# Kernel tuning notes

Measured on AMD Instinct MI355X. Metric: run time of the kernel, lower is better.

## Reference

```python
import jax, jax.numpy as jnp
import numpy as np
from jax import lax

SR = 4      # sr_ratio
HEADS = 8   # num_heads


def _upsample_bilinear_ac(x, out_h, out_w):
    # torch nn.Upsample(scale_factor=SR, mode='bilinear', align_corners=True)
    B, C, h, w = x.shape
    ys = jnp.linspace(0.0, h - 1.0, out_h)
    xs = jnp.linspace(0.0, w - 1.0, out_w)
    y0 = jnp.floor(ys).astype(jnp.int32)
    y1 = jnp.minimum(y0 + 1, h - 1)
    wy = (ys - y0).astype(x.dtype)
    x0 = jnp.floor(xs).astype(jnp.int32)
    x1 = jnp.minimum(x0 + 1, w - 1)
    wx = (xs - x0).astype(x.dtype)
    r = x[:, :, y0, :] * (1.0 - wy)[None, None, :, None] + x[:, :, y1, :] * wy[None, None, :, None]
    return r[:, :, :, x0] * (1.0 - wx) + r[:, :, :, x1] * wx


def _forward(x, sr_w, sr_b, ln_g, ln_b, q_w, k1_w, v1_w, k2_w, v2_w, proj_w, proj_b):
    B, C, H, W = x.shape
    ID = C // 4                      # internal_dim
    hd = ID // HEADS                 # head_dim
    scale = float(hd) ** -0.5
    # spatial-reduction conv for Q path: [B, ID, H/4, W/4]
    qf = lax.conv_general_dilated(x, sr_w, (SR, SR), 'VALID',
                                  dimension_numbers=('NCHW', 'OIHW', 'NCHW'))
    qf = qf + sr_b[None, :, None, None]
    Hs, Ws = qf.shape[2], qf.shape[3]
    N = Hs * Ws
    qf = qf.reshape(B, ID, N).transpose(0, 2, 1)          # [B, N, ID]
    # LayerNorm
    mu = qf.mean(-1, keepdims=True)
    var = qf.var(-1, keepdims=True)
    qn = (qf - mu) / jnp.sqrt(var + 1e-5) * ln_g + ln_b
    q = qn @ q_w                                          # [B, N, ID]
    # max / avg pooled K,V inputs: [B, N, C]
    xm = lax.reduce_window(x, -jnp.inf, lax.max, (1, 1, SR, SR), (1, 1, SR, SR), 'VALID')
    xm = xm.reshape(B, C, N).transpose(0, 2, 1)
    xa = lax.reduce_window(x, 0.0, lax.add, (1, 1, SR, SR), (1, 1, SR, SR), 'VALID') / float(SR * SR)
    xa = xa.reshape(B, C, N).transpose(0, 2, 1)

    def heads(t):
        return t.reshape(B, N, HEADS, hd).transpose(0, 2, 1, 3)  # [B, H, N, hd]

    qh = heads(q)
    k1, v1 = heads(xm @ k1_w), heads(xm @ v1_w)
    k2, v2 = heads(xa @ k2_w), heads(xa @ v2_w)

    def attend(k, v):
        a = jax.nn.softmax(jnp.einsum('bhnd,bhmd->bhnm', qh, k) * scale, axis=-1)
        return jnp.einsum('bhnm,bhmd->bhnd', a, v)

    z = attend(k1, v1) + attend(k2, v2)                   # [B, H, N, hd]
    z = z.transpose(0, 2, 1, 3).reshape(B, N, ID)
    z = z @ proj_w + proj_b                               # [B, N, C]
    z = z.transpose(0, 2, 1).reshape(B, C, Hs, Ws)
    return _upsample_bilinear_ac(z, H, W)


def setup_inputs() -> dict:
    key = jax.random.key(0)
    ks = jax.random.split(key, 9)
    B, C, H, W = 16, 256, 112, 112
    ID = C // 4

    def n(k, shape, s=0.02):
        return jax.random.normal(k, shape, jnp.float32) * s

    return {
        'x': jax.random.normal(ks[0], (B, C, H, W), jnp.float32),
        'sr_w': n(ks[1], (ID, C, SR, SR)),
        'sr_b': jnp.zeros((ID,), jnp.float32),
        'ln_g': jnp.ones((ID,), jnp.float32),
        'ln_b': jnp.zeros((ID,), jnp.float32),
        'q_w': n(ks[2], (ID, ID)),
        'k1_w': n(ks[3], (C, ID)),
        'v1_w': n(ks[4], (C, ID)),
        'k2_w': n(ks[5], (C, ID)),
        'v2_w': n(ks[6], (C, ID)),
        'proj_w': n(ks[7], (ID, C)),
        'proj_b': jnp.zeros((C,), jnp.float32),
    }


def reference(x, sr_w, sr_b, ln_g, ln_b, q_w, k1_w, v1_w, k2_w, v2_w, proj_w, proj_b):
    return _forward(x, sr_w, sr_b, ln_g, ln_b, q_w, k1_w, v1_w, k2_w, v2_w, proj_w, proj_b)
```

## Files before the change

kernel.cpp:

```cpp
#include <hip/hip_runtime.h>
#include <math.h>

typedef __attribute__((ext_vector_type(8))) short short8;
typedef __attribute__((ext_vector_type(4))) short bh4;
typedef __attribute__((ext_vector_type(4))) float f32x4;
typedef __attribute__((ext_vector_type(2))) unsigned uint2v;
typedef __attribute__((ext_vector_type(4))) unsigned uint4v;

#define MFMA16(A,B,C) __builtin_amdgcn_mfma_f32_16x16x32_bf16(A,B,C,0,0,0)

#if __has_builtin(__builtin_amdgcn_mfma_f32_16x16x16bf16_1k)
#define MFMA16x16(A,B,C) __builtin_amdgcn_mfma_f32_16x16x16bf16_1k(A,B,C,0,0,0)
#else
__device__ __forceinline__ f32x4 mfma16x16_asm(bh4 a, bh4 b, f32x4 c){
    asm volatile("v_mfma_f32_16x16x16_bf16 %0, %1, %2, %0" : "+v"(c) : "v"(a), "v"(b));
    return c;
}
#define MFMA16x16(A,B,C) mfma16x16_asm(A,B,C)
#endif

__device__ __forceinline__ unsigned short f2b(float f){
    unsigned u = __builtin_bit_cast(unsigned, f);
    return (unsigned short)((u + 0x7fffu + ((u>>16)&1u)) >> 16);
}
__device__ __forceinline__ unsigned pk2(float a, float b){
    return (unsigned)f2b(a) | ((unsigned)f2b(b) << 16);
}
__device__ __forceinline__ unsigned pk2rn(float a, float b){
    unsigned ua = __builtin_bit_cast(unsigned, a) + 0x8000u;
    unsigned ub = __builtin_bit_cast(unsigned, b) + 0x8000u;
    return (ua >> 16) | (ub & 0xffff0000u);
}
__device__ __forceinline__ void gl_lds16(const void* g, void* l){
    __builtin_amdgcn_global_load_lds(
        (const __attribute__((address_space(1))) void*)g,
        (__attribute__((address_space(3))) void*)l, 16, 0, 0);
}


__global__ __launch_bounds__(256) void ktw(const float* __restrict__ srw,
    const float* __restrict__ qw, const float* __restrict__ k1w,
    const float* __restrict__ v1w, const float* __restrict__ k2w,
    const float* __restrict__ v2w, char* __restrict__ srwb,
    char* __restrict__ Wtm, char* __restrict__ Wta, char* __restrict__ QWt)
{
    int blk = blockIdx.x, t = threadIdx.x;
    if (blk < 128){
        int base = blk*2048 + t*8;
        float4 a = *(const float4*)(srw + base);
        float4 b = *(const float4*)(srw + base + 4);
        uint4 u = { pk2(a.x,a.y), pk2(a.z,a.w), pk2(b.x,b.y), pk2(b.z,b.w) };
        *(uint4*)(srwb + (size_t)base*2) = u;
    } else if (blk < 136){
        __shared__ float T[256*33];
        int idx = blk - 128, fi = idx >> 1, half = idx & 1;
        const float* src = (fi==0) ? k1w : (fi==1) ? v1w : (fi==2) ? k2w : v2w;
        char* dst = ((fi < 2) ? Wtm : Wta) + (size_t)((fi & 1)*64 + half*32) * 512;
        for (int li = t; li < 8192; li += 256){
            int c = li >> 5, o = li & 31;
            T[c*33 + o] = src[c*64 + half*32 + o];
        }
        __syncthreads();
        for (int lo = t; lo < 1024; lo += 256){
            int o = lo >> 5, c8 = lo & 31;
            float v[8];
            #pragma unroll
            for (int k = 0; k < 8; ++k) v[k] = T[(c8*8 + k)*33 + o];
            uint4 u = { pk2(v[0],v[1]), pk2(v[2],v[3]), pk2(v[4],v[5]), pk2(v[6],v[7]) };
            *(uint4*)(dst + o*512 + c8*16) = u;
        }
    } else {
        __shared__ float T[64*65];
        for (int li = t; li < 4096; li += 256)
            T[(li >> 6)*65 + (li & 63)] = qw[li];
        __syncthreads();
        for (int lo = t; lo < 512; lo += 256){
            int o = lo >> 3, i8 = lo & 7;
            float v[8];
            #pragma unroll
            for (int k = 0; k < 8; ++k) v[k] = T[(i8*8 + k)*65 + o];
            uint4 u = { pk2(v[0],v[1]), pk2(v[2],v[3]), pk2(v[4],v[5]), pk2(v[6],v[7]) };
            *(uint4*)(QWt + o*128 + i8*16) = u;
        }
    }
}

__global__ __launch_bounds__(256) void k1(const float* __restrict__ x,
    const char* __restrict__ srwb, char* __restrict__ R, float* __restrict__ pws)
{
    __shared__ __align__(16) char Xb0[14336];
    __shared__ __align__(16) char Xb1[14336];
    __shared__ __align__(16) char Xb2[14336];
    __shared__ unsigned pmpa[28*66];
    int blk = blockIdx.x;
    int b = blk / 112, r5 = blk % 112, hs = r5 >> 2, cg4 = r5 & 3;
    int t = threadIdx.x;
    int w = t >> 6, l = t & 63, lr = l & 15, lg = l >> 4;
    int p0 = lr, p1m = min(16 + lr, 27);
    int nIss = (w < 3) ? 4 : 2;
    int jbase = (w < 3) ? w*4 : 12;

    size_t gchunk[4]; int ldso[4];
    #pragma unroll
    for (int q = 0; q < 4; ++q){
        int byte_in = (jbase + q)*1024 + l*16;
        int c = byte_in / 1792, rem = byte_in - c*1792;
        gchunk[q] = (size_t)c*50176 + rem;
        ldso[q] = (jbase + q)*1024;
    }
    const char* xstage = (const char*)x
        + ((size_t)(b*256 + cg4*64)*12544 + (size_t)hs*448)*4;
    const char* bRow = srwb + (size_t)(w*16 + lr)*8192 + cg4*2048 + lg*16;
    int pl_p = t >> 3, pl_c = t & 7;

    f32x4 acc0 = {0.f,0.f,0.f,0.f}, acc1 = {0.f,0.f,0.f,0.f};
    short8 Q00,Q01,Q02,Q03, Q10,Q11,Q12,Q13, Q20,Q21,Q22,Q23;

#define BPRE(B0,B1,B2,B3,S) do{ \
    B0 = *(const short8*)(bRow + (S)*256);      \
    B1 = *(const short8*)(bRow + (S)*256 + 64); \
    B2 = *(const short8*)(bRow + (S)*256 + 128);\
    B3 = *(const short8*)(bRow + (S)*256 + 192); }while(0)

#define STAGE(XB,S) do{ \
    const char* _gb = xstage + (size_t)(S)*401408; \
    _Pragma("unroll") for (int q = 0; q < 4; ++q){ \
        if (q < nIss) gl_lds16(_gb + gchunk[q], XB + ldso[q]); } }while(0)

#define WAIT16 do{ if (w < 3) asm volatile("s_waitcnt vmcnt(16)" ::: "memory"); \
                   else       asm volatile("s_waitcnt vmcnt(12)" ::: "memory"); \
                   __builtin_amdgcn_sched_barrier(0); }while(0)
#define WAIT8  do{ if (w < 3) asm volatile("s_waitcnt vmcnt(8)" ::: "memory"); \
                   else       asm volatile("s_waitcnt vmcnt(6)" ::: "memory"); \
                   __builtin_amdgcn_sched_barrier(0); }while(0)
#define WAIT0  do{ asm volatile("s_waitcnt vmcnt(0)" ::: "memory"); \
                   __builtin_amdgcn_sched_barrier(0); }while(0)
#define BAR    do{ __builtin_amdgcn_s_barrier(); __builtin_amdgcn_sched_barrier(0); }while(0)

#define COMP(XB,B0,B1,B2,B3,S) do{ \
    if (t < 224){ \
        const char* cb = XB + pl_c*1792 + pl_p*16; \
        f32x4 r0 = *(const f32x4*)(cb);        f32x4 r1 = *(const f32x4*)(cb + 448); \
        f32x4 r2 = *(const f32x4*)(cb + 896);  f32x4 r3 = *(const f32x4*)(cb + 1344); \
        float mx = fmaxf(fmaxf(fmaxf(r0[0],r0[1]),fmaxf(r0[2],r0[3])), \
                         fmaxf(fmaxf(r1[0],r1[1]),fmaxf(r1[2],r1[3]))); \
        mx = fmaxf(mx, fmaxf(fmaxf(fmaxf(r2[0],r2[1]),fmaxf(r2[2],r2[3])), \
                             fmaxf(fmaxf(r3[0],r3[1]),fmaxf(r3[2],r3[3])))); \
        float sm = ((r0[0]+r0[1])+(r0[2]+r0[3])) + ((r1[0]+r1[1])+(r1[2]+r1[3])) \
                 + ((r2[0]+r2[1])+(r2[2]+r2[3])) + ((r3[0]+r3[1])+(r3[2]+r3[3])); \
        pmpa[pl_p*66 + (S)*8 + pl_c] = pk2(mx, sm * (1.f/16.f)); \
    } \
    _Pragma("unroll") for (int ks = 0; ks < 4; ++ks){ \
        const char* abase = XB + (ks*2 + (lg>>1))*1792 + (lg&1)*896; \
        f32x4 lo0 = *(const f32x4*)(abase + p0*16); \
        f32x4 hi0 = *(const f32x4*)(abase + 448 + p0*16); \
        f32x4 lo1 = *(const f32x4*)(abase + p1m*16); \
        f32x4 hi1 = *(const f32x4*)(abase + 448 + p1m*16); \
        short8 af0 = __builtin_bit_cast(short8, \
            (uint4v){ pk2(lo0[0],lo0[1]), pk2(lo0[2],lo0[3]), pk2(hi0[0],hi0[1]), pk2(hi0[2],hi0[3]) }); \
        short8 af1 = __builtin_bit_cast(short8, \
            (uint4v){ pk2(lo1[0],lo1[1]), pk2(lo1[2],lo1[3]), pk2(hi1[0],hi1[1]), pk2(hi1[2],hi1[3]) }); \
        short8 bq = (ks==0)?B0:(ks==1)?B1:(ks==2)?B2:B3; \
        acc0 = MFMA16(af0, bq, acc0); \
        acc1 = MFMA16(af1, bq, acc1); } }while(0)

    BPRE(Q00,Q01,Q02,Q03, 0); STAGE(Xb0, 0);
    BPRE(Q10,Q11,Q12,Q13, 1); STAGE(Xb1, 1);
    BPRE(Q20,Q21,Q22,Q23, 2); STAGE(Xb2, 2);

    WAIT16; BAR; COMP(Xb0, Q00,Q01,Q02,Q03, 0); BAR;
    BPRE(Q00,Q01,Q02,Q03, 3); STAGE(Xb0, 3);
    WAIT16; BAR; COMP(Xb1, Q10,Q11,Q12,Q13, 1); BAR;
    BPRE(Q10,Q11,Q12,Q13, 4); STAGE(Xb1, 4);
    WAIT16; BAR; COMP(Xb2, Q20,Q21,Q22,Q23, 2); BAR;
    BPRE(Q20,Q21,Q22,Q23, 5); STAGE(Xb2, 5);
    WAIT16; BAR; COMP(Xb0, Q00,Q01,Q02,Q03, 3); BAR;
    BPRE(Q00,Q01,Q02,Q03, 6); STAGE(Xb0, 6);
    WAIT16; BAR; COMP(Xb1, Q10,Q11,Q12,Q13, 4); BAR;
    BPRE(Q10,Q11,Q12,Q13, 7); STAGE(Xb1, 7);
    WAIT16; BAR; COMP(Xb2, Q20,Q21,Q22,Q23, 5); BAR;
    WAIT8;  BAR; COMP(Xb0, Q00,Q01,Q02,Q03, 6); BAR;
    WAIT0;  BAR; COMP(Xb1, Q10,Q11,Q12,Q13, 7);

#undef BPRE
#undef STAGE
#undef WAIT16
#undef WAIT8
#undef WAIT0
#undef BAR
#undef COMP

    size_t rowB = (size_t)b*784 + hs*28;
    float* pp = pws + (size_t)((b*28 + hs)*4 + cg4)*1792;
    #pragma unroll
    for (int rg = 0; rg < 4; ++rg){
        int m0 = lg*4 + rg, m1 = 16 + lg*4 + rg;
        pp[m0*64 + w*16 + lr] = acc0[rg];
        if (m1 < 28) pp[m1*64 + w*16 + lr] = acc1[rg];
    }
    __syncthreads();
    if (t < 224){
        int m = t >> 3, sub = t & 7;
        unsigned u[8];
        #pragma unroll
        for (int k = 0; k < 8; ++k) u[k] = pmpa[m*66 + sub*8 + k];
        uint4 um = { (u[0]&0xffffu)|(u[1]<<16), (u[2]&0xffffu)|(u[3]<<16),
                     (u[4]&0xffffu)|(u[5]<<16), (u[6]&0xffffu)|(u[7]<<16) };
        uint4 ua = { (u[0]>>16)|(u[1]&0xffff0000u), (u[2]>>16)|(u[3]&0xffff0000u),
                     (u[4]>>16)|(u[5]&0xffff0000u), (u[6]>>16)|(u[7]&0xffff0000u) };
        *(uint4*)(R + (rowB + m)*1024 + cg4*128 + sub*16)       = um;
        *(uint4*)(R + (rowB + m)*1024 + 512 + cg4*128 + sub*16) = ua;
    }
}

__global__ __launch_bounds__(512) void k2(const float* __restrict__ pws_,
    const float* __restrict__ srb, const float* __restrict__ lng,
    const float* __restrict__ lnb, const char* __restrict__ Wtm,
    const char* __restrict__ Wta, const char* __restrict__ QWt,
    char* __restrict__ R)
{
    __shared__ __align__(16) char PM[16384];
    __shared__ __align__(16) char PA[16384];
    __shared__ float Db[32*64];
    __shared__ __align__(16) char QN[4096];
    int blk = blockIdx.x, b = blk/28, hs = blk%28;
    int t = threadIdx.x, w = t>>6, l = t&63, lr = l&15, lg = l>>4;
    size_t rowB = (size_t)b*784 + hs*28;
    const char* Rb = R + rowB*1024;
    for (int li = t; li < 896; li += 512){
        int m = li >> 5, c16 = li & 31;
        uint4 vm = *(const uint4*)(Rb + (size_t)m*1024 + c16*16);
        uint4 va = *(const uint4*)(Rb + (size_t)m*1024 + 512 + c16*16);
        int dst = m*512 + ((c16*16) ^ ((m&7)<<4));
        *(uint4*)(PM + dst) = vm;
        *(uint4*)(PA + dst) = va;
    }
    const float* p0 = pws_ + (size_t)(b*28 + hs)*4*1792;
    for (int e = t; e < 1792; e += 512)
        Db[e] = ((p0[e] + p0[1792+e]) + (p0[3584+e] + p0[5376+e])) + srb[e & 63];
    __syncthreads();
    float g = lng[l], be = lnb[l];
    #pragma unroll
    for (int i = 0; i < 4; ++i){
        int m = w + i*8;
        float v = Db[m*64 + l];
        float s = v, ss = v*v;
        #pragma unroll
        for (int off = 1; off < 64; off <<= 1){
            s  += __shfl_xor(s,  off, 64);
            ss += __shfl_xor(ss, off, 64);
        }
        float mu = s * (1.f/64.f);
        float var = ss * (1.f/64.f) - mu*mu;
        float qn = (v - mu) * rsqrtf(var + 1e-5f) * g + be;
        *(unsigned short*)(QN + m*128 + ((l*2) ^ ((m&7)<<4))) = f2b(qn);
    }
    __syncthreads();
    int fam = w >> 2, ofp = w & 3;
    const char* PMA = fam ? PA : PM;
    const char* Wt  = fam ? Wta : Wtm;
    f32x4 a00={0.f,0.f,0.f,0.f}, a01=a00, a10=a00, a11=a00;
    int swzr = (lr & 7) << 4;
    #pragma unroll
    for (int ks = 0; ks < 8; ++ks){
        int kb = ks*64 + lg*16;
        short8 x0 = *(const short8*)(PMA + lr*512 + (kb ^ swzr));
        short8 x1 = *(const short8*)(PMA + (16+lr)*512 + (kb ^ swzr));
        short8 b0 = *(const short8*)(Wt + (size_t)(ofp*32 + lr)*512 + kb);
        short8 b1 = *(const short8*)(Wt + (size_t)(ofp*32 + 16 + lr)*512 + kb);
        a00 = MFMA16(x0, b0, a00); a01 = MFMA16(x0, b1, a01);
        a10 = MFMA16(x1, b0, a10); a11 = MFMA16(x1, b1, a11);
    }
    f32x4 q0={0.f,0.f,0.f,0.f}, q1=q0;
    if (w < 4){
        #pragma unroll
        for (int ks = 0; ks < 2; ++ks){
            int kb = ks*64 + lg*16;
            short8 xa_ = *(const short8*)(QN + lr*128 + (kb ^ swzr));
            short8 xb_ = *(const short8*)(QN + (16+lr)*128 + (kb ^ swzr));
            short8 bq  = *(const short8*)(QWt + (size_t)(w*16 + lr)*128 + kb);
            q0 = MFMA16(xa_, bq, q0);
            q1 = MFMA16(xb_, bq, q1);
        }
    }
    #pragma unroll
    for (int j = 0; j < 2; ++j){
        int o128 = ofp*32 + j*16 + lr;
        int o = o128 & 63, hh = o >> 3, dd = o & 7, mat = fam*2 + (o128 >> 6);
        int byteoff = 128 + hh*64 + mat*16 + dd*2;
        f32x4 am  = j ? a01 : a00;
        f32x4 am1 = j ? a11 : a10;
        #pragma unroll
        for (int rg = 0; rg < 4; ++rg){
            int m0 = lg*4 + rg, m1 = 16 + lg*4 + rg;
            *(unsigned short*)(R + (rowB + m0)*1024 + byteoff) = f2b(am[rg]);
            if (m1 < 28)
                *(unsigned short*)(R + (rowB + m1)*1024 + byteoff) = f2b(am1[rg]);
        }
    }
    if (w < 4){
        int o = w*16 + lr;
        #pragma unroll
        for (int rg = 0; rg < 4; ++rg){
            int m0 = lg*4 + rg, m1 = 16 + lg*4 + rg;
            *(unsigned short*)(R + (rowB + m0)*1024 + o*2) = f2b(q0[rg]);
            if (m1 < 28)
                *(unsigned short*)(R + (rowB + m1)*1024 + o*2) = f2b(q1[rg]);
        }
    }
}

__global__ __launch_bounds__(256) void kattn(const char* __restrict__ R, float* __restrict__ z)
{
    __shared__ __align__(16) char QT [6144];
    __shared__ __align__(16) char K1b[5376];
    __shared__ __align__(16) char K2b[5376];
    __shared__ __align__(16) char VT1[3840];
    __shared__ __align__(16) char VT2[3840];
    int blk = blockIdx.x;
    int bh = blk / 7, nseg = blk % 7;
    int b = bh >> 3, h = bh & 7;
    int t = threadIdx.x, w = t >> 6, l = t & 63;
    int col = l & 15, g = l >> 4;

    for (int i = t; i < 384; i += 256) ((uint4*)QT)[i] = uint4{0,0,0,0};
    for (int i = t; i < 112; i += 256){
        *(uint4*)(K1b + i*48 + 16) = uint4{0,0,0,0};
        *(uint4*)(K2b + i*48 + 16) = uint4{0,0,0,0};
    }
    for (int i = t; i < 120; i += 256){
        *(uint4*)(VT1 + 1920 + i*16) = uint4{0,0,0,0};
        *(uint4*)(VT2 + 1920 + i*16) = uint4{0,0,0,0};
    }
    __syncthreads();
    if (t < 112){
        uint4 qv = *(const uint4*)(R + ((size_t)b*784 + nseg*112 + t)*1024 + h*16);
        *(uint2*)(QT + t*48)     = uint2{qv.x, qv.y};
        *(uint2*)(QT + t*48 + 8) = uint2{qv.z, qv.w};
    }
    __syncthreads();

    bh4 qf[2];
    #pragma unroll
    for (int nf = 0; nf < 2; ++nf)
        qf[nf] = *(const bh4*)(QT + (w*28 + nf*16 + col)*48 + g*8);

    f32x4 o1[2] = {{0,0,0,0},{0,0,0,0}}, o2[2] = {{0,0,0,0},{0,0,0,0}};
    float d1[2] = {0.f,0.f}, d2[2] = {0.f,0.f};
    const float C2 = 0.51004244f;

    for (int mt = 0; mt < 7; ++mt){
        __syncthreads();
        for (int li = t; li < 448; li += 256){
            int m = li >> 2, part = li & 3;
            uint4 v = *(const uint4*)(R + ((size_t)b*784 + mt*112 + m)*1024 + 128 + h*64 + part*16);
            if ((part & 1) == 0){
                char* Kb = (part == 0) ? K1b : K2b;
                *(uint2*)(Kb + m*48)     = uint2{v.x, v.y};
                *(uint2*)(Kb + m*48 + 8) = uint2{v.z, v.w};
            } else {
                char* Vb = (part == 1) ? VT1 : VT2;
                unsigned arr[4] = {v.x, v.y, v.z, v.w};
                #pragma unroll
                for (int d = 0; d < 4; ++d){
                    *(unsigned short*)(Vb + (d*2)*240   + m*2) = (unsigned short)(arr[d] & 0xffffu);
                    *(unsigned short*)(Vb + (d*2+1)*240 + m*2) = (unsigned short)(arr[d] >> 16);
                }
            }
        }
        __syncthreads();
        #pragma unroll
        for (int mc = 0; mc < 7; ++mc){
            bh4 ka = *(const bh4*)(K1b + (mc*16 + col)*48 + g*8);
            bh4 kb = *(const bh4*)(K2b + (mc*16 + col)*48 + g*8);
            bh4 va = *(const bh4*)(VT1 + col*240 + mc*32 + g*8);
            bh4 vb = *(const bh4*)(VT2 + col*240 + mc*32 + g*8);
            #pragma unroll
            for (int nf = 0; nf < 2; ++nf){
                f32x4 zr = {0.f,0.f,0.f,0.f};
                f32x4 s1 = MFMA16x16(ka, qf[nf], zr);
                float p0 = exp2f(s1[0]*C2), p1 = exp2f(s1[1]*C2);
                float p2 = exp2f(s1[2]*C2), p3 = exp2f(s1[3]*C2);
                d1[nf] += (p0+p1)+(p2+p3);
                bh4 pf1 = __builtin_bit_cast(bh4, (uint2v){pk2rn(p0,p1), pk2rn(p2,p3)});
                o1[nf] = MFMA16x16(va, pf1, o1[nf]);
                f32x4 s2 = MFMA16x16(kb, qf[nf], zr);
                float r0 = exp2f(s2[0]*C2), r1 = exp2f(s2[1]*C2);
                float r2 = exp2f(s2[2]*C2), r3 = exp2f(s2[3]*C2);
                d2[nf] += (r0+r1)+(r2+r3);
                bh4 pf2 = __builtin_bit_cast(bh4, (uint2v){pk2rn(r0,r1), pk2rn(r2,r3)});
                o2[nf] = MFMA16x16(vb, pf2, o2[nf]);
            }
        }
    }
    #pragma unroll
    for (int nf = 0; nf < 2; ++nf){
        d1[nf] += __shfl_xor(d1[nf], 16, 64); d1[nf] += __shfl_xor(d1[nf], 32, 64);
        d2[nf] += __shfl_xor(d2[nf], 16, 64); d2[nf] += __shfl_xor(d2[nf], 32, 64);
    }
    if (g < 2){
        #pragma unroll
        for (int nf = 0; nf < 2; ++nf){
            if (nf == 1 && col >= 12) continue;
            int n = nseg*112 + w*28 + nf*16 + col;
            float ra = 1.f / d1[nf], rb = 1.f / d2[nf];
            float4 ov;
            ov.x = o1[nf][0]*ra + o2[nf][0]*rb;
            ov.y = o1[nf][1]*ra + o2[nf][1]*rb;
            ov.z = o1[nf][2]*ra + o2[nf][2]*rb;
            ov.w = o1[nf][3]*ra + o2[nf][3]*rb;
            *(float4*)(z + ((size_t)b*784 + n)*64 + h*8 + g*4) = ov;
        }
    }
}

__global__ __launch_bounds__(256) void kpu(const float* __restrict__ z,
    const float* __restrict__ pw, const float* __restrict__ pb,
    float* __restrict__ out)
{
    __shared__ float plane[8*784];
    __shared__ float wsl[64*8];
    __shared__ int   ti0[112];
    __shared__ float twv[112];
    int blk = blockIdx.x;
    int b = blk >> 5, cg = blk & 31;
    int t = threadIdx.x;
    if (t < 128){
        #pragma unroll
        for (int q = 0; q < 4; ++q){
            int idx = t*4 + q; int o = idx >> 3, j = idx & 7;
            wsl[o*8 + j] = pw[o*256 + cg*8 + j];
        }
    }
    if (t < 112){
        float s = (float)t * (27.f/111.f);
        int i0 = (int)s; if (i0 > 27) i0 = 27;
        ti0[t] = i0; twv[t] = s - (float)i0;
    }
    __syncthreads();
    {
        int nh = t >> 1, jh = (t & 1) * 4;
        float bias0 = pb[cg*8 + jh], bias1 = pb[cg*8 + jh + 1];
        float bias2 = pb[cg*8 + jh + 2], bias3 = pb[cg*8 + jh + 3];
        for (int n = nh; n < 784; n += 128){
            const float* zr = z + ((size_t)b*784 + n)*64;
            float a0 = bias0, a1 = bias1, a2 = bias2, a3 = bias3;
            #pragma unroll
            for (int o4 = 0; o4 < 16; ++o4){
                float4 zv = *(const float4*)(zr + o4*4);
                const float* wr = wsl + (o4*4)*8 + jh;
                a0 = fmaf(zv.x, wr[0],  a0); a1 = fmaf(zv.x, wr[1],  a1);
                a2 = fmaf(zv.x, wr[2],  a2); a3 = fmaf(zv.x, wr[3],  a3);
                a0 = fmaf(zv.y, wr[8],  a0); a1 = fmaf(zv.y, wr[9],  a1);
                a2 = fmaf(zv.y, wr[10], a2); a3 = fmaf(zv.y, wr[11], a3);
                a0 = fmaf(zv.z, wr[16], a0); a1 = fmaf(zv.z, wr[17], a1);
                a2 = fmaf(zv.z, wr[18], a2); a3 = fmaf(zv.z, wr[19], a3);
                a0 = fmaf(zv.w, wr[24], a0); a1 = fmaf(zv.w, wr[25], a1);
                a2 = fmaf(zv.w, wr[26], a2); a3 = fmaf(zv.w, wr[27], a3);
            }
            plane[(jh+0)*784 + n] = a0;
            plane[(jh+1)*784 + n] = a1;
            plane[(jh+2)*784 + n] = a2;
            plane[(jh+3)*784 + n] = a3;
        }
    }
    __syncthreads();
    float* ob = out + ((size_t)b*256 + cg*8)*12544;
    for (int i = t; i < 12544; i += 256){
        int y = i/112, xx = i%112;
        int y0 = ti0[y], x0 = ti0[xx];
        float wy = twv[y], wx = twv[xx];
        int y1 = min(y0+1, 27), x1 = min(x0+1, 27);
        int i00 = y0*28 + x0, i01 = y0*28 + x1, i10 = y1*28 + x0, i11 = y1*28 + x1;
        #pragma unroll
        for (int j = 0; j < 8; ++j){
            const float* pl = plane + j*784;
            float a  = pl[i00] + (pl[i10]-pl[i00])*wy;
            float bb = pl[i01] + (pl[i11]-pl[i01])*wy;
            ob[(size_t)j*12544 + i] = a + (bb-a)*wx;
        }
    }
}

extern "C" void kernel_launch(void* const* d_in, const int* in_sizes, int n_in,
                              void* d_out, int out_size, void* d_ws, size_t ws_size,
                              hipStream_t stream) {
    const float* x   = (const float*)d_in[0];
    const float* srw = (const float*)d_in[1];
    const float* srb = (const float*)d_in[2];
    const float* lng = (const float*)d_in[3];
    const float* lnb = (const float*)d_in[4];
    const float* qw  = (const float*)d_in[5];
    const float* k1w = (const float*)d_in[6];
    const float* v1w = (const float*)d_in[7];
    const float* k2w = (const float*)d_in[8];
    const float* v2w = (const float*)d_in[9];
    const float* pw  = (const float*)d_in[10];
    const float* pb  = (const float*)d_in[11];

    char*  Rws  = (char*)d_ws;
    float* pws  = (float*)(Rws + 12845056);
    char*  srwb = Rws + 25690112;
    char*  Wtm  = Rws + 26214400;
    char*  Wta  = Rws + 26279936;
    char*  QWt  = Rws + 26345472;
    float* z    = (float*)(Rws + 12845056);
    float* out  = (float*)d_out;

    ktw  <<<137,  256, 0, stream>>>(srw, qw, k1w, v1w, k2w, v2w, srwb, Wtm, Wta, QWt);
    k1   <<<1792, 256, 0, stream>>>(x, srwb, Rws, pws);
    k2   <<<448,  512, 0, stream>>>(pws, srb, lng, lnb, Wtm, Wta, QWt, Rws);
    kattn<<<896,  256, 0, stream>>>(Rws, z);
    kpu  <<<512,  256, 0, stream>>>(z, pw, pb, out);
}
```

Before: 233.6 us.

## Split k1 conv reduction across waves and XOR-swizzle LDS staging

Each wave in k1 now handles one K-slice (two channels) for all 64 output channels, instead of all K-slices for 16 output channels. Each wave does 8 MFMAs per stage from one A-fragment load, which cuts redundant LDS A reads and bf16 conversions. The global-to-LDS layout gets an XOR swizzle on the 16-byte column to reduce LDS bank conflicts. The cost is four times as many accumulator registers, and the per-wave partial sums must be reduced through LDS with extra barriers before the store.

```diff
diff --git a/kernel.cpp b/kernel.cpp
--- a/kernel.cpp
+++ b/kernel.cpp
@@ -88,9 +88,7 @@
 __global__ __launch_bounds__(256) void k1(const float* __restrict__ x,
     const char* __restrict__ srwb, char* __restrict__ R, float* __restrict__ pws)
 {
-    __shared__ __align__(16) char Xb0[14336];
-    __shared__ __align__(16) char Xb1[14336];
-    __shared__ __align__(16) char Xb2[14336];
+    __shared__ __align__(16) char Xb[3][14336];
     __shared__ unsigned pmpa[28*66];
     int blk = blockIdx.x;
     int b = blk / 112, r5 = blk % 112, hs = r5 >> 2, cg4 = r5 & 3;
@@ -105,27 +103,34 @@
     for (int q = 0; q < 4; ++q){
         int byte_in = (jbase + q)*1024 + l*16;
         int c = byte_in / 1792, rem = byte_in - c*1792;
-        gchunk[q] = (size_t)c*50176 + rem;
+        gchunk[q] = (size_t)c*50176 + (size_t)(rem ^ ((c & 7) << 4));
         ldso[q] = (jbase + q)*1024;
     }
     const char* xstage = (const char*)x
         + ((size_t)(b*256 + cg4*64)*12544 + (size_t)hs*448)*4;
-    const char* bRow = srwb + (size_t)(w*16 + lr)*8192 + cg4*2048 + lg*16;
+    const char* bBase = srwb + (size_t)lr*8192 + cg4*2048 + w*64 + lg*16;
     int pl_p = t >> 3, pl_c = t & 7;
-
-    f32x4 acc0 = {0.f,0.f,0.f,0.f}, acc1 = {0.f,0.f,0.f,0.f};
-    short8 Q00,Q01,Q02,Q03, Q10,Q11,Q12,Q13, Q20,Q21,Q22,Q23;
+    int kxp = pl_c << 4;
+    int chA = 2*w + (lg >> 1);
+    int kxA = chA << 4;
+    int remA0 = (lg & 1)*896 + p0*16;
+    int remA1 = (lg & 1)*896 + p1m*16;
+
+    f32x4 acc00={0.f,0.f,0.f,0.f}, acc01=acc00, acc02=acc00, acc03=acc00;
+    f32x4 acc10=acc00, acc11=acc00, acc12=acc00, acc13=acc00;
+    short8 P00,P01,P02,P03, P10,P11,P12,P13, P20,P21,P22,P23;
 
 #define BPRE(B0,B1,B2,B3,S) do{ \
-    B0 = *(const short8*)(bRow + (S)*256);      \
-    B1 = *(const short8*)(bRow + (S)*256 + 64); \
-    B2 = *(const short8*)(bRow + (S)*256 + 128);\
-    B3 = *(const short8*)(bRow + (S)*256 + 192); }while(0)
-
-#define STAGE(XB,S) do{ \
+    B0 = *(const short8*)(bBase + (S)*256);            \
+    B1 = *(const short8*)(bBase + (S)*256 + 131072);   \
+    B2 = *(const short8*)(bBase + (S)*256 + 262144);   \
+    B3 = *(const short8*)(bBase + (S)*256 + 393216); }while(0)
+
+#define STAGE(BI,S) do{ \
     const char* _gb = xstage + (size_t)(S)*401408; \
+    char* _xb = &Xb[BI][0]; \
     _Pragma("unroll") for (int q = 0; q < 4; ++q){ \
-        if (q < nIss) gl_lds16(_gb + gchunk[q], XB + ldso[q]); } }while(0)
+        if (q < nIss) gl_lds16(_gb + gchunk[q], _xb + ldso[q]); } }while(0)
 
 #define WAIT16 do{ if (w < 3) asm volatile("s_waitcnt vmcnt(16)" ::: "memory"); \
                    else       asm volatile("s_waitcnt vmcnt(12)" ::: "memory"); \
@@ -137,11 +142,15 @@
                    __builtin_amdgcn_sched_barrier(0); }while(0)
 #define BAR    do{ __builtin_amdgcn_s_barrier(); __builtin_amdgcn_sched_barrier(0); }while(0)
 
-#define COMP(XB,B0,B1,B2,B3,S) do{ \
+#define COMP(BI,B0,B1,B2,B3,S) do{ \
+    const char* _XB = &Xb[BI][0]; \
     if (t < 224){ \
-        const char* cb = XB + pl_c*1792 + pl_p*16; \
-        f32x4 r0 = *(const f32x4*)(cb);        f32x4 r1 = *(const f32x4*)(cb + 448); \
-        f32x4 r2 = *(const f32x4*)(cb + 896);  f32x4 r3 = *(const f32x4*)(cb + 1344); \
+        const char* cbch = _XB + pl_c*1792; \
+        int rb = pl_p*16; \
+        f32x4 r0 = *(const f32x4*)(cbch + ((rb)        ^ kxp)); \
+        f32x4 r1 = *(const f32x4*)(cbch + ((rb + 448)  ^ kxp)); \
+        f32x4 r2 = *(const f32x4*)(cbch + ((rb + 896)  ^ kxp)); \
+        f32x4 r3 = *(const f32x4*)(cbch + ((rb + 1344) ^ kxp)); \
         float mx = fmaxf(fmaxf(fmaxf(r0[0],r0[1]),fmaxf(r0[2],r0[3])), \
                          fmaxf(fmaxf(r1[0],r1[1]),fmaxf(r1[2],r1[3]))); \
         mx = fmaxf(mx, fmaxf(fmaxf(fmaxf(r2[0],r2[1]),fmaxf(r2[2],r2[3])), \
@@ -150,37 +159,39 @@
                  + ((r2[0]+r2[1])+(r2[2]+r2[3])) + ((r3[0]+r3[1])+(r3[2]+r3[3])); \
         pmpa[pl_p*66 + (S)*8 + pl_c] = pk2(mx, sm * (1.f/16.f)); \
     } \
-    _Pragma("unroll") for (int ks = 0; ks < 4; ++ks){ \
-        const char* abase = XB + (ks*2 + (lg>>1))*1792 + (lg&1)*896; \
-        f32x4 lo0 = *(const f32x4*)(abase + p0*16); \
-        f32x4 hi0 = *(const f32x4*)(abase + 448 + p0*16); \
-        f32x4 lo1 = *(const f32x4*)(abase + p1m*16); \
-        f32x4 hi1 = *(const f32x4*)(abase + 448 + p1m*16); \
+    { \
+        const char* abch = _XB + chA*1792; \
+        f32x4 lo0 = *(const f32x4*)(abch + ((remA0)       ^ kxA)); \
+        f32x4 hi0 = *(const f32x4*)(abch + ((remA0 + 448) ^ kxA)); \
+        f32x4 lo1 = *(const f32x4*)(abch + ((remA1)       ^ kxA)); \
+        f32x4 hi1 = *(const f32x4*)(abch + ((remA1 + 448) ^ kxA)); \
         short8 af0 = __builtin_bit_cast(short8, \
             (uint4v){ pk2(lo0[0],lo0[1]), pk2(lo0[2],lo0[3]), pk2(hi0[0],hi0[1]), pk2(hi0[2],hi0[3]) }); \
         short8 af1 = __builtin_bit_cast(short8, \
             (uint4v){ pk2(lo1[0],lo1[1]), pk2(lo1[2],lo1[3]), pk2(hi1[0],hi1[1]), pk2(hi1[2],hi1[3]) }); \
-        short8 bq = (ks==0)?B0:(ks==1)?B1:(ks==2)?B2:B3; \
-        acc0 = MFMA16(af0, bq, acc0); \
-        acc1 = MFMA16(af1, bq, acc1); } }while(0)
-
-    BPRE(Q00,Q01,Q02,Q03, 0); STAGE(Xb0, 0);
-    BPRE(Q10,Q11,Q12,Q13, 1); STAGE(Xb1, 1);
-    BPRE(Q20,Q21,Q22,Q23, 2); STAGE(Xb2, 2);
-
-    WAIT16; BAR; COMP(Xb0, Q00,Q01,Q02,Q03, 0); BAR;
-    BPRE(Q00,Q01,Q02,Q03, 3); STAGE(Xb0, 3);
-    WAIT16; BAR; COMP(Xb1, Q10,Q11,Q12,Q13, 1); BAR;
-    BPRE(Q10,Q11,Q12,Q13, 4); STAGE(Xb1, 4);
-    WAIT16; BAR; COMP(Xb2, Q20,Q21,Q22,Q23, 2); BAR;
-    BPRE(Q20,Q21,Q22,Q23, 5); STAGE(Xb2, 5);
-    WAIT16; BAR; COMP(Xb0, Q00,Q01,Q02,Q03, 3); BAR;
-    BPRE(Q00,Q01,Q02,Q03, 6); STAGE(Xb0, 6);
-    WAIT16; BAR; COMP(Xb1, Q10,Q11,Q12,Q13, 4); BAR;
-    BPRE(Q10,Q11,Q12,Q13, 7); STAGE(Xb1, 7);
-    WAIT16; BAR; COMP(Xb2, Q20,Q21,Q22,Q23, 5); BAR;
-    WAIT8;  BAR; COMP(Xb0, Q00,Q01,Q02,Q03, 6); BAR;
-    WAIT0;  BAR; COMP(Xb1, Q10,Q11,Q12,Q13, 7);
+        acc00 = MFMA16(af0, B0, acc00); acc01 = MFMA16(af0, B1, acc01); \
+        acc02 = MFMA16(af0, B2, acc02); acc03 = MFMA16(af0, B3, acc03); \
+        acc10 = MFMA16(af1, B0, acc10); acc11 = MFMA16(af1, B1, acc11); \
+        acc12 = MFMA16(af1, B2, acc12); acc13 = MFMA16(af1, B3, acc13); \
+    } }while(0)
+
+    BPRE(P00,P01,P02,P03, 0); STAGE(0, 0);
+    BPRE(P10,P11,P12,P13, 1); STAGE(1, 1);
+    BPRE(P20,P21,P22,P23, 2); STAGE(2, 2);
+
+    WAIT16; BAR; COMP(0, P00,P01,P02,P03, 0); BAR;
+    BPRE(P00,P01,P02,P03, 3); STAGE(0, 3);
+    WAIT16; BAR; COMP(1, P10,P11,P12,P13, 1); BAR;
+    BPRE(P10,P11,P12,P13, 4); STAGE(1, 4);
+    WAIT16; BAR; COMP(2, P20,P21,P22,P23, 2); BAR;
+    BPRE(P20,P21,P22,P23, 5); STAGE(2, 5);
+    WAIT16; BAR; COMP(0, P00,P01,P02,P03, 3); BAR;
+    BPRE(P00,P01,P02,P03, 6); STAGE(0, 6);
+    WAIT16; BAR; COMP(1, P10,P11,P12,P13, 4); BAR;
+    BPRE(P10,P11,P12,P13, 7); STAGE(1, 7);
+    WAIT16; BAR; COMP(2, P20,P21,P22,P23, 5); BAR;
+    WAIT8;  BAR; COMP(0, P00,P01,P02,P03, 6); BAR;
+    WAIT0;  BAR; COMP(1, P10,P11,P12,P13, 7);
 
 #undef BPRE
 #undef STAGE
@@ -190,15 +201,30 @@
 #undef BAR
 #undef COMP
 
+    __syncthreads();
+    {
+        float* wb = (float*)(&Xb[0][0]) + w*2048;
+        #pragma unroll
+        for (int rg = 0; rg < 4; ++rg){
+            int m0 = lg*4 + rg, m1 = 16 + lg*4 + rg;
+            wb[m0*64 + lr]      = acc00[rg];
+            wb[m0*64 + 16 + lr] = acc01[rg];
+            wb[m0*64 + 32 + lr] = acc02[rg];
+            wb[m0*64 + 48 + lr] = acc03[rg];
+            wb[m1*64 + lr]      = acc10[rg];
+            wb[m1*64 + 16 + lr] = acc11[rg];
+            wb[m1*64 + 32 + lr] = acc12[rg];
+            wb[m1*64 + 48 + lr] = acc13[rg];
+        }
+    }
+    __syncthreads();
     size_t rowB = (size_t)b*784 + hs*28;
-    float* pp = pws + (size_t)((b*28 + hs)*4 + cg4)*1792;
-    #pragma unroll
-    for (int rg = 0; rg < 4; ++rg){
-        int m0 = lg*4 + rg, m1 = 16 + lg*4 + rg;
-        pp[m0*64 + w*16 + lr] = acc0[rg];
-        if (m1 < 28) pp[m1*64 + w*16 + lr] = acc1[rg];
-    }
-    __syncthreads();
+    {
+        const float* Xf = (const float*)(&Xb[0][0]);
+        float* pp = pws + (size_t)((b*28 + hs)*4 + cg4)*1792;
+        for (int e = t; e < 1792; e += 256)
+            pp[e] = (Xf[e] + Xf[2048 + e]) + (Xf[4096 + e] + Xf[6144 + e]);
+    }
     if (t < 224){
         int m = t >> 3, sub = t & 7;
         unsigned u[8];
```

Measured after the change: 237.7 us. About the same (+1.8%).
